# Optimization experiments

Hardware: AMD Instinct MI355X
Metric: run time of the kernel (lower is better)

Reference implementation:

```python
import jax, jax.numpy as jnp
import numpy as np

E4M3_MAX = 448.0  # max finite value of float8_e4m3fn
EQN = "btd,df->btf"


def compute_scale(amax, scale, fp8_max):
    # flax fp8_ops.compute_scale: `scale` is the dequant scale (scale_inv in TE terms)
    sf = fp8_max / amax
    sf = jnp.where(amax > 0.0, sf, 1.0 / scale)
    sf = jnp.where(jnp.isfinite(amax), sf, 1.0 / scale)
    return 1.0 / sf


def compute_amax_history(x, history):
    amax = jnp.max(jnp.abs(x)).astype(history.dtype)
    return jnp.roll(history, shift=-1, axis=0).at[0].set(amax)


def quantize_dequantize(x, q_dtype, scale, compute_dtype, fp8_max):
    scaled = x / scale.astype(compute_dtype)
    clipped = jnp.clip(scaled, -fp8_max, fp8_max)
    q = clipped.astype(q_dtype)
    return q.astype(compute_dtype) * scale.astype(compute_dtype)


def in_qdq_math(x, scale, history, q_dtype, fp8_max, compute_dtype):
    # flax fp8_ops.in_qdq forward: update amax history, recompute scale, qdq with new scale
    new_history = compute_amax_history(x, history)
    amax_from_history = jnp.max(new_history)
    new_scale = compute_scale(amax_from_history, scale, fp8_max)
    qx = quantize_dequantize(x, q_dtype, new_scale, compute_dtype, fp8_max)
    return qx, new_scale, new_history


def setup_inputs() -> dict:
    key = jax.random.key(0)
    kx, kk = jax.random.split(key)
    B, T, D, F, H = 8, 8192, 256, 256, 1024
    return {
        "x": jax.random.normal(kx, (B, T, D), jnp.float32),
        "k": jax.random.normal(kk, (D, F), jnp.float32),
        "input_scale": jnp.ones((1,), jnp.float32),
        "kernel_scale": jnp.ones((1,), jnp.float32),
        "output_grad_scale": jnp.ones((1,), jnp.float32),
        "input_amax_history": jnp.zeros((H,), jnp.float32),
        "kernel_amax_history": jnp.zeros((H,), jnp.float32),
        "output_grad_amax_history": jnp.zeros((H,), jnp.float32),
    }


def reference(x, k, input_scale, kernel_scale, output_grad_scale,
              input_amax_history, kernel_amax_history, output_grad_amax_history):
    comp = jnp.float32
    x = x.astype(comp)
    k = k.astype(comp)
    x_qdq, _, _ = in_qdq_math(x, input_scale, input_amax_history,
                              jnp.float8_e4m3fn, E4M3_MAX, comp)
    k_qdq, _, _ = in_qdq_math(k, kernel_scale, kernel_amax_history,
                              jnp.float8_e4m3fn, E4M3_MAX, comp)
    # dot_general_with_precision just runs lax.dot_general with default precision
    y = jnp.einsum(EQN, x_qdq, k_qdq)  # [B, T, F]
    # out_qdq is the identity in the forward pass (it qdq's only the gradient)
    return y
```

## Files before the change

### kernel.cpp

```cpp
#include <hip/hip_runtime.h>
#include <stdint.h>

#define FP8_MAX 448.0f
#define NXB 2048

typedef __attribute__((ext_vector_type(4))) float f32x4;
typedef long long ll;

__device__ __forceinline__ float scale_factor(float amax, float prev_scale) {
    float sf = FP8_MAX / amax;
    if (!(amax > 0.0f) || !isfinite(amax)) sf = 1.0f / prev_scale;
    return sf;
}

__device__ __forceinline__ unsigned pack4_fp8(float a, float b, float c, float d) {
    int v = __builtin_amdgcn_cvt_pk_fp8_f32(a, b, 0, false);
    v = __builtin_amdgcn_cvt_pk_fp8_f32(c, d, v, true);
    return (unsigned)v;
}

__device__ __forceinline__ float amax4(f32x4 v, float m) {
    float a0 = fmaxf(__builtin_fabsf(v.x), __builtin_fabsf(v.y));
    float a1 = fmaxf(__builtin_fabsf(v.z), __builtin_fabsf(v.w));
    return fmaxf(m, fmaxf(a0, a1));
}

__global__ __launch_bounds__(256) void prep_kernel(
    const float* __restrict__ x, const float* __restrict__ k,
    const float* __restrict__ kernel_scale,
    float* __restrict__ partials, float* __restrict__ kamaxf,
    ll* __restrict__ pack) {
    __shared__ float sm[4];
    int tid = threadIdx.x;
    int lane = tid & 63, w = tid >> 6;

    if (blockIdx.x != 0) {
        const f32x4* p = (const f32x4*)x;
        unsigned base = (blockIdx.x - 1) * 256 + tid;
        float m = 0.0f;
        #pragma unroll
        for (int t = 0; t < 8; ++t)
            m = amax4(p[base + (unsigned)t * (NXB * 256)], m);
        #pragma unroll
        for (int off = 32; off; off >>= 1)
            m = fmaxf(m, __shfl_down(m, off, 64));
        if (lane == 0) sm[w] = m;
        __syncthreads();
        if (tid == 0)
            partials[blockIdx.x - 1] =
                fmaxf(fmaxf(sm[0], sm[1]), fmaxf(sm[2], sm[3]));
    } else {
        const f32x4* p = (const f32x4*)k;
        float m = 0.0f;
        #pragma unroll 8
        for (int t = 0; t < 64; ++t)
            m = amax4(p[tid + t * 256], m);
        #pragma unroll
        for (int off = 32; off; off >>= 1)
            m = fmaxf(m, __shfl_down(m, off, 64));
        if (lane == 0) sm[w] = m;
        __syncthreads();
        float amax = fmaxf(fmaxf(sm[0], sm[1]), fmaxf(sm[2], sm[3]));
        if (tid == 0) kamaxf[0] = amax;
        float sf = scale_factor(amax, kernel_scale[0]);
        for (int i = 0; i < 32; ++i) {
            int t = tid + i * 256;
            int l = t & 63;
            int nt = (t >> 6) & 15;
            int kstep = t >> 10;
            int col = nt * 16 + (l & 15);
            int k0 = kstep * 32 + (l >> 4) * 8;
            float v[8];
            #pragma unroll
            for (int j = 0; j < 8; ++j)
                v[j] = k[(k0 + j) * 256 + col] * sf;
            unsigned lo = pack4_fp8(v[0], v[1], v[2], v[3]);
            unsigned hi = pack4_fp8(v[4], v[5], v[6], v[7]);
            pack[t] = (ll)lo | ((ll)hi << 32);
        }
    }
}

__global__ __launch_bounds__(256, 3) void gemm_kernel(
    const float* __restrict__ x, const ll* __restrict__ Bpack,
    const float* __restrict__ partials, const float* __restrict__ kamaxf,
    const float* __restrict__ input_scale, const float* __restrict__ kernel_scale,
    float* __restrict__ C) {
    __shared__ char ldsc[32 * 256];

    int tid = threadIdx.x;
    int w = tid >> 6;
    int lane = tid & 63;
    int kg = lane >> 4, r16 = lane & 15;

    const float* xt = x + (size_t)blockIdx.x * 32 * 256;
    f32x4 raw[8];
    #pragma unroll
    for (int i = 0; i < 8; ++i) {
        const float* p = xt + i * 1024 + tid * 4;
        asm volatile("global_load_dwordx4 %0, %1, off"
                     : "=v"(raw[i]) : "v"(p) : "memory");
    }

    ll Breg[32];
    #pragma unroll
    for (int i = 0; i < 32; ++i)
        Breg[i] = Bpack[(i >> 2) * 1024 + (w * 4 + (i & 3)) * 64 + lane];

    const f32x4* pp = (const f32x4*)partials;
    float m = 0.0f;
    #pragma unroll
    for (int i = 0; i < 8; ++i)
        m = amax4(pp[lane + i * 64], m);
    #pragma unroll
    for (int off = 32; off; off >>= 1)
        m = fmaxf(m, __shfl_xor(m, off, 64));
    float sf_x = scale_factor(m, input_scale[0]);
    float sf_k = scale_factor(kamaxf[0], kernel_scale[0]);
    float outscale = (1.0f / sf_x) * (1.0f / sf_k);

    asm volatile("s_waitcnt vmcnt(0)" ::: "memory");
    __builtin_amdgcn_sched_barrier(0);
    #pragma unroll
    for (int i = 0; i < 8; ++i) {
        int row = i * 4 + w;
        int col = lane * 4;
        unsigned v = pack4_fp8(raw[i].x * sf_x, raw[i].y * sf_x,
                               raw[i].z * sf_x, raw[i].w * sf_x);
        *(unsigned*)&ldsc[row * 256 + (col ^ ((row & 15) << 3))] = v;
    }
    __syncthreads();

    float* cbase = C + (size_t)blockIdx.x * 32 * 256 + w * 64;
    #pragma unroll
    for (int rg = 0; rg < 2; ++rg) {
        int row = rg * 16 + r16;
        unsigned rbase = (unsigned)row * 256;
        unsigned sw = (unsigned)(r16 << 3);
        ll A[8];
        #pragma unroll
        for (int ks = 0; ks < 8; ++ks)
            A[ks] = *(const ll*)&ldsc[rbase + (((unsigned)(kg * 8 + ks * 32)) ^ sw)];

        f32x4 acc[4];
        #pragma unroll
        for (int j = 0; j < 4; ++j) acc[j] = (f32x4){0.f, 0.f, 0.f, 0.f};
        #pragma unroll
        for (int ks = 0; ks < 8; ++ks)
            #pragma unroll
            for (int j = 0; j < 4; ++j)
                acc[j] = __builtin_amdgcn_mfma_f32_16x16x32_fp8_fp8(
                    A[ks], Breg[ks * 4 + j], acc[j], 0, 0, 0);

        int crow = rg * 16 + kg * 4;
        #pragma unroll
        for (int j = 0; j < 4; ++j)
            #pragma unroll
            for (int r = 0; r < 4; ++r)
                cbase[(size_t)(crow + r) * 256 + j * 16 + r16] =
                    acc[j][r] * outscale;
    }
}

extern "C" void kernel_launch(void* const* d_in, const int* in_sizes, int n_in,
                              void* d_out, int out_size, void* d_ws, size_t ws_size,
                              hipStream_t stream) {
    const float* x = (const float*)d_in[0];
    const float* k = (const float*)d_in[1];
    const float* input_scale = (const float*)d_in[2];
    const float* kernel_scale = (const float*)d_in[3];
    float* out = (float*)d_out;

    float* partials = (float*)d_ws;
    float* kamaxf = partials + 2048;
    ll* pack = (ll*)((char*)d_ws + 16384);

    int nx = in_sizes[0];
    int M = nx / 256;

    prep_kernel<<<NXB + 1, 256, 0, stream>>>(x, k, kernel_scale,
                                             partials, kamaxf, pack);
    gemm_kernel<<<M / 32, 256, 0, stream>>>(x, pack, partials, kamaxf,
                                            input_scale, kernel_scale, out);
}
```

Measured before the change: 48.20 us.

## Split kernel packing across blocks, contiguous x amax, swapped MFMA for vector stores

```diff
diff --git a/kernel.cpp b/kernel.cpp
--- a/kernel.cpp
+++ b/kernel.cpp
@@ -2,6 +2,7 @@
 #include <stdint.h>
 
 #define FP8_MAX 448.0f
+#define KBLK 16
 #define NXB 2048
 
 typedef __attribute__((ext_vector_type(4))) float f32x4;
@@ -34,21 +35,20 @@
     int tid = threadIdx.x;
     int lane = tid & 63, w = tid >> 6;
 
-    if (blockIdx.x != 0) {
-        const f32x4* p = (const f32x4*)x;
-        unsigned base = (blockIdx.x - 1) * 256 + tid;
+    if (blockIdx.x >= KBLK) {
+        unsigned xb = blockIdx.x - KBLK;
+        const f32x4* p = (const f32x4*)x + (size_t)xb * 2048;
         float m = 0.0f;
         #pragma unroll
         for (int t = 0; t < 8; ++t)
-            m = amax4(p[base + (unsigned)t * (NXB * 256)], m);
+            m = amax4(p[tid + t * 256], m);
         #pragma unroll
         for (int off = 32; off; off >>= 1)
             m = fmaxf(m, __shfl_down(m, off, 64));
         if (lane == 0) sm[w] = m;
         __syncthreads();
         if (tid == 0)
-            partials[blockIdx.x - 1] =
-                fmaxf(fmaxf(sm[0], sm[1]), fmaxf(sm[2], sm[3]));
+            partials[xb] = fmaxf(fmaxf(sm[0], sm[1]), fmaxf(sm[2], sm[3]));
     } else {
         const f32x4* p = (const f32x4*)k;
         float m = 0.0f;
@@ -63,8 +63,9 @@
         float amax = fmaxf(fmaxf(sm[0], sm[1]), fmaxf(sm[2], sm[3]));
         if (tid == 0) kamaxf[0] = amax;
         float sf = scale_factor(amax, kernel_scale[0]);
-        for (int i = 0; i < 32; ++i) {
-            int t = tid + i * 256;
+        #pragma unroll
+        for (int ii = 0; ii < 2; ++ii) {
+            int t = (blockIdx.x * 2 + ii) * 256 + tid;
             int l = t & 63;
             int nt = (t >> 6) & 15;
             int kstep = t >> 10;
@@ -86,21 +87,13 @@
     const float* __restrict__ partials, const float* __restrict__ kamaxf,
     const float* __restrict__ input_scale, const float* __restrict__ kernel_scale,
     float* __restrict__ C) {
-    __shared__ char ldsc[32 * 256];
+    __shared__ char lds[32 * 256];
 
     int tid = threadIdx.x;
     int w = tid >> 6;
     int lane = tid & 63;
     int kg = lane >> 4, r16 = lane & 15;
-
-    const float* xt = x + (size_t)blockIdx.x * 32 * 256;
-    f32x4 raw[8];
-    #pragma unroll
-    for (int i = 0; i < 8; ++i) {
-        const float* p = xt + i * 1024 + tid * 4;
-        asm volatile("global_load_dwordx4 %0, %1, off"
-                     : "=v"(raw[i]) : "v"(p) : "memory");
-    }
+    unsigned sw = (unsigned)(r16 << 3);
 
     ll Breg[32];
     #pragma unroll
@@ -119,28 +112,39 @@
     float sf_k = scale_factor(kamaxf[0], kernel_scale[0]);
     float outscale = (1.0f / sf_x) * (1.0f / sf_k);
 
+    asm volatile("s_waitcnt vmcnt(0) lgkmcnt(0)" ::: "memory");
+    __builtin_amdgcn_sched_barrier(0);
+
+    const float* xt = x + (size_t)blockIdx.x * 32 * 256;
+    f32x4 raw[8];
+    #pragma unroll
+    for (int i = 0; i < 8; ++i) {
+        const float* p = xt + i * 1024 + tid * 4;
+        asm volatile("global_load_dwordx4 %0, %1, off"
+                     : "=v"(raw[i]) : "v"(p) : "memory");
+    }
     asm volatile("s_waitcnt vmcnt(0)" ::: "memory");
     __builtin_amdgcn_sched_barrier(0);
+
     #pragma unroll
     for (int i = 0; i < 8; ++i) {
         int row = i * 4 + w;
-        int col = lane * 4;
         unsigned v = pack4_fp8(raw[i].x * sf_x, raw[i].y * sf_x,
                                raw[i].z * sf_x, raw[i].w * sf_x);
-        *(unsigned*)&ldsc[row * 256 + (col ^ ((row & 15) << 3))] = v;
+        *(unsigned*)&lds[row * 256 + ((lane * 4) ^ ((row & 15) << 3))] = v;
     }
-    __syncthreads();
+    asm volatile("s_waitcnt lgkmcnt(0)" ::: "memory");
+    __builtin_amdgcn_s_barrier();
+    __builtin_amdgcn_sched_barrier(0);
 
-    float* cbase = C + (size_t)blockIdx.x * 32 * 256 + w * 64;
+    float* cb = C + (size_t)blockIdx.x * 32 * 256 + w * 64;
     #pragma unroll
     for (int rg = 0; rg < 2; ++rg) {
-        int row = rg * 16 + r16;
-        unsigned rbase = (unsigned)row * 256;
-        unsigned sw = (unsigned)(r16 << 3);
+        unsigned rbase = (unsigned)((rg * 16 + r16) * 256);
         ll A[8];
         #pragma unroll
         for (int ks = 0; ks < 8; ++ks)
-            A[ks] = *(const ll*)&ldsc[rbase + (((unsigned)(kg * 8 + ks * 32)) ^ sw)];
+            A[ks] = *(const ll*)&lds[rbase + (((unsigned)(kg * 8 + ks * 32)) ^ sw)];
 
         f32x4 acc[4];
         #pragma unroll
@@ -150,15 +154,13 @@
             #pragma unroll
             for (int j = 0; j < 4; ++j)
                 acc[j] = __builtin_amdgcn_mfma_f32_16x16x32_fp8_fp8(
-                    A[ks], Breg[ks * 4 + j], acc[j], 0, 0, 0);
+                    Breg[ks * 4 + j], A[ks], acc[j], 0, 0, 0);
 
-        int crow = rg * 16 + kg * 4;
         #pragma unroll
-        for (int j = 0; j < 4; ++j)
-            #pragma unroll
-            for (int r = 0; r < 4; ++r)
-                cbase[(size_t)(crow + r) * 256 + j * 16 + r16] =
-                    acc[j][r] * outscale;
+        for (int j = 0; j < 4; ++j) {
+            f32x4 o = acc[j] * outscale;
+            *(f32x4*)&cb[(size_t)(rg * 16 + r16) * 256 + j * 16 + kg * 4] = o;
+        }
     }
 }
 
@@ -172,14 +174,14 @@
     float* out = (float*)d_out;
 
     float* partials = (float*)d_ws;
-    float* kamaxf = partials + 2048;
+    float* kamaxf = (float*)((char*)d_ws + 12288);
     ll* pack = (ll*)((char*)d_ws + 16384);
 
     int nx = in_sizes[0];
     int M = nx / 256;
 
-    prep_kernel<<<NXB + 1, 256, 0, stream>>>(x, k, kernel_scale,
-                                             partials, kamaxf, pack);
+    prep_kernel<<<NXB + KBLK, 256, 0, stream>>>(x, k, kernel_scale,
+                                                partials, kamaxf, pack);
     gemm_kernel<<<M / 32, 256, 0, stream>>>(x, pack, partials, kamaxf,
                                             input_scale, kernel_scale, out);
 }
```

Result: faster. 44.59 us (-7.5%).
